# Performance work log

Measured on AMD Instinct MI355X. Metric: run time of the kernel, lower is better.

The kernel has to match this reference:

```python
import jax, jax.numpy as jnp
import numpy as np
from jax.scipy.special import logsumexp

B, S, T = 512, 512, 78  # batch, seq_len, num_tags (num_types=78 in SatoModel)


def setup_inputs() -> dict:
    key = jax.random.key(0)
    k1, k2, k3, k4, k5 = jax.random.split(key, 5)
    emissions = jax.random.normal(k1, (B, S, T), dtype=jnp.float32)
    mask = jax.random.randint(k2, (B, S), 0, 2).astype(bool)
    start_transitions = jax.random.normal(k3, (T,), dtype=jnp.float32)
    end_transitions = jax.random.normal(k4, (T,), dtype=jnp.float32)
    transitions = jax.random.normal(k5, (T, T), dtype=jnp.float32)
    return {
        "emissions": emissions,
        "mask": mask,
        "start_transitions": start_transitions,
        "end_transitions": end_transitions,
        "transitions": transitions,
    }


def reference(emissions, mask, start_transitions, end_transitions, transitions):
    # CRF.forward: partition - score
    # score: masked forward algorithm (note: this CRF's _compute_score never uses
    # gold tags; it is a masked logsumexp DP, reproduced faithfully).
    # partition: unmasked forward algorithm (its where(mask, a, a) is a no-op).
    init = start_transitions[None, :] + emissions[:, 0]  # [B, T]

    ems = jnp.moveaxis(emissions[:, 1:], 1, 0)  # [S-1, B, T]
    msk = jnp.moveaxis(mask[:, 1:], 1, 0)       # [S-1, B]

    def dp_step(state, em_i):
        # state: [B, T]; transitions: [T, T]; em_i: [B, T]
        return logsumexp(state[:, :, None] + transitions[None, :, :] + em_i[:, None, :], axis=1)

    def step(carry, inp):
        score, alpha = carry
        em_i, m_i = inp
        next_score = dp_step(score, em_i)
        score = jnp.where(m_i[:, None], next_score, score)
        alpha = dp_step(alpha, em_i)
        return (score, alpha), None

    (score, alpha), _ = jax.lax.scan(step, (init, init), (ems, msk))

    score_final = logsumexp(score + end_transitions[None, :], axis=1)      # [B]
    partition = logsumexp(alpha + end_transitions[None, :], axis=1)        # [B]
    return partition - score_final
```

## Files before the change

kernel.cpp:

```cpp
#include <hip/hip_runtime.h>

#define BB 256
#define SS 512
#define TT 78
#define TP 80
#define NT 256

typedef float v2f __attribute__((ext_vector_type(2)));
typedef float v4f __attribute__((ext_vector_type(4)));

template<int I> struct ic { static constexpr int v = I; };
template<int I, int N, typename F>
__device__ __forceinline__ void sfor(F f) {
    if constexpr (I < N) { f(ic<I>{}); sfor<I + 1, N>(f); }
}

__global__ __attribute__((amdgpu_flat_work_group_size(NT, NT)))
void crf_fwd_kernel(const float* __restrict__ em,
                    const unsigned int* __restrict__ mi32,
                    const float* __restrict__ st,
                    const float* __restrict__ en_,
                    const float* __restrict__ tr,
                    float* __restrict__ out)
{
    __shared__ __align__(16) float sE[4][TP];
    __shared__ float sfin[4];
    __shared__ int sflag;
    __shared__ char lds_pad[84 * 1024];

    const int tid  = threadIdx.x;
    const int w    = tid >> 6;
    const int lane = tid & 63;
    ((volatile char*)lds_pad)[tid] = 0;

    const int  batch    = blockIdx.x * 2 + (w >> 1);
    const bool is_alpha = (w & 1) != 0;
    const bool has2     = lane < (TT - 64);
    const int  t0  = lane;
    const int  t1c = has2 ? (lane + 64) : (TT - 1);

    if (tid == 0) sflag = 1;
    __syncthreads();
    { bool ok = true;
      for (int k = tid; k < 512; k += NT) ok = ok && (mi32[k] <= 1u);
      if (!ok) atomicAnd(&sflag, 0); }
    __syncthreads();
    const bool mask_int = (sflag != 0);
    const unsigned char* mi8 = (const unsigned char*)mi32;

    v2f et0[TP / 2], et1[TP / 2];
    sfor<0, TP / 2>([&](auto P) {
        constexpr int p = decltype(P)::v;
        constexpr int j0 = 2 * p, j1 = 2 * p + 1;
        float a0v = (j0 < TT) ? __expf(tr[j0 * TT + t0])  : 0.f;
        float a1v = (j1 < TT) ? __expf(tr[j1 * TT + t0])  : 0.f;
        float b0v = (j0 < TT) ? __expf(tr[j0 * TT + t1c]) : 0.f;
        float b1v = (j1 < TT) ? __expf(tr[j1 * TT + t1c]) : 0.f;
        asm volatile("" : "+v"(a0v), "+v"(a1v), "+v"(b0v), "+v"(b1v));
        et0[p] = (v2f){a0v, a1v};
        et1[p] = (v2f){b0v, b1v};
    });

    const size_t base = (size_t)batch * SS * TT;
    float e0 = __expf(st[t0]  + em[base + t0]);
    float e1 = __expf(st[t1c] + em[base + t1c]);
    int M2 = 0;

    if (lane == 14 || lane == 15) sE[w][64 + lane] = 0.f;
    sE[w][lane] = e0;
    if (has2) sE[w][64 + lane] = e1;

    const float* rp = em + base + TT;
    float EmN0 = __expf(rp[t0]);
    float EmN1 = __expf(rp[t1c]);
    unsigned int mk_n = mask_int ? mi32[batch * SS + 1]
                                 : (unsigned int)mi8[batch * SS + 1];

    for (int i = 1; i < SS; ++i) {
        const float Em0 = EmN0, Em1 = EmN1;
        const unsigned int mki = mk_n;
        if (i + 1 < SS) {
            rp += TT;
            EmN0 = __expf(rp[t0]);
            EmN1 = __expf(rp[t1c]);
            mk_n = mask_int ? mi32[batch * SS + i + 1]
                            : (unsigned int)mi8[batch * SS + i + 1];
        }
        __builtin_amdgcn_wave_barrier();

        const v4f* ep = (const v4f*)sE[w];
        v4f xs[TP / 4];
        sfor<0, TP / 4>([&](auto K) { constexpr int k = decltype(K)::v; xs[k] = ep[k]; });

        v2f a0{0,0}, a1{0,0}, c0{0,0}, c1{0,0};
        sfor<0, TP / 4>([&](auto K) {
            constexpr int k = decltype(K)::v;
            v2f xlo = {xs[k].x, xs[k].y}, xhi = {xs[k].z, xs[k].w};
            a0 = __builtin_elementwise_fma(xlo, et0[2 * k],     a0);
            a1 = __builtin_elementwise_fma(xhi, et0[2 * k + 1], a1);
            c0 = __builtin_elementwise_fma(xlo, et1[2 * k],     c0);
            c1 = __builtin_elementwise_fma(xhi, et1[2 * k + 1], c1);
        });
        v2f va = a0 + a1, vc = c0 + c1;
        float v0 = va.x + va.y;
        float v1 = vc.x + vc.y;

        float vref = __builtin_amdgcn_readfirstlane(v0);
        int   d2   = (int)((__float_as_uint(vref) >> 23) & 0xFF) - 127;
        float scl  = __uint_as_float((unsigned)(127 - d2) << 23);
        float n0 = v0 * scl * Em0;
        float n1 = v1 * scl * Em1;

        const bool upd = is_alpha | (mki != 0);
        e0 = upd ? n0 : e0;
        e1 = upd ? n1 : e1;
        M2 = upd ? M2 + d2 : M2;

        __builtin_amdgcn_wave_barrier();
        sE[w][lane] = e0;
        if (has2) sE[w][64 + lane] = e1;
    }

    float fs = e0 * __expf(en_[t0]);
    if (has2) fs += e1 * __expf(en_[t1c]);
    #pragma unroll
    for (int o = 32; o > 0; o >>= 1) fs += __shfl_xor(fs, o);
    if (lane == 0) sfin[w] = __logf(fs) + (float)M2 * 0.6931471805599453f;
    __syncthreads();
    if (tid == 0) {
        out[blockIdx.x * 2 + 0] = sfin[1] - sfin[0];
        out[blockIdx.x * 2 + 1] = sfin[3] - sfin[2];
    }
}

extern "C" void kernel_launch(void* const* d_in, const int* in_sizes, int n_in,
                              void* d_out, int out_size, void* d_ws, size_t ws_size,
                              hipStream_t stream) {
    const float* emissions    = (const float*)d_in[0];
    const unsigned int* mask  = (const unsigned int*)d_in[1];
    const float* start_trans  = (const float*)d_in[2];
    const float* end_trans    = (const float*)d_in[3];
    const float* transitions  = (const float*)d_in[4];
    float* out = (float*)d_out;

    crf_fwd_kernel<<<BB, NT, 0, stream>>>(emissions, mask, start_trans,
                                          end_trans, transitions, out);
}
```

Baseline: 201.1 us.

## Use packed fp16 dot2 for CRF transition matvec with one batch per block

```diff
diff --git a/kernel.cpp b/kernel.cpp
--- a/kernel.cpp
+++ b/kernel.cpp
@@ -1,13 +1,12 @@
 #include <hip/hip_runtime.h>
 
-#define BB 256
+#define BB 512
 #define SS 512
 #define TT 78
 #define TP 80
-#define NT 256
+#define NT 128
 
-typedef float v2f __attribute__((ext_vector_type(2)));
-typedef float v4f __attribute__((ext_vector_type(4)));
+typedef _Float16 v2h __attribute__((ext_vector_type(2)));
 
 template<int I> struct ic { static constexpr int v = I; };
 template<int I, int N, typename F>
@@ -15,7 +14,12 @@
     if constexpr (I < N) { f(ic<I>{}); sfor<I + 1, N>(f); }
 }
 
-__global__ __attribute__((amdgpu_flat_work_group_size(NT, NT)))
+__device__ __forceinline__ unsigned short f16b(float x) {
+    return __builtin_bit_cast(unsigned short, (_Float16)x);
+}
+
+__global__ __attribute__((amdgpu_flat_work_group_size(NT, NT),
+                          amdgpu_waves_per_eu(1, 1)))
 void crf_fwd_kernel(const float* __restrict__ em,
                     const unsigned int* __restrict__ mi32,
                     const float* __restrict__ st,
@@ -23,21 +27,17 @@
                     const float* __restrict__ tr,
                     float* __restrict__ out)
 {
-    __shared__ __align__(16) float sE[4][TP];
-    __shared__ float sfin[4];
-    __shared__ int sflag;
-    __shared__ char lds_pad[84 * 1024];
-
+    const int b    = blockIdx.x;
     const int tid  = threadIdx.x;
     const int w    = tid >> 6;
     const int lane = tid & 63;
-    ((volatile char*)lds_pad)[tid] = 0;
-
-    const int  batch    = blockIdx.x * 2 + (w >> 1);
-    const bool is_alpha = (w & 1) != 0;
-    const bool has2     = lane < (TT - 64);
+    const bool has2 = lane < (TT - 64);
     const int  t0  = lane;
     const int  t1c = has2 ? (lane + 64) : (TT - 1);
+
+    __shared__ __align__(16) unsigned short sEh[2][TP];
+    __shared__ float sfin[2];
+    __shared__ int sflag;
 
     if (tid == 0) sflag = 1;
     __syncthreads();
@@ -47,34 +47,36 @@
     __syncthreads();
     const bool mask_int = (sflag != 0);
     const unsigned char* mi8 = (const unsigned char*)mi32;
+    const bool is_alpha = (w == 1);
 
-    v2f et0[TP / 2], et1[TP / 2];
+    unsigned wt0[TP / 2], wt1[TP / 2];
     sfor<0, TP / 2>([&](auto P) {
         constexpr int p = decltype(P)::v;
         constexpr int j0 = 2 * p, j1 = 2 * p + 1;
-        float a0v = (j0 < TT) ? __expf(tr[j0 * TT + t0])  : 0.f;
-        float a1v = (j1 < TT) ? __expf(tr[j1 * TT + t0])  : 0.f;
-        float b0v = (j0 < TT) ? __expf(tr[j0 * TT + t1c]) : 0.f;
-        float b1v = (j1 < TT) ? __expf(tr[j1 * TT + t1c]) : 0.f;
-        asm volatile("" : "+v"(a0v), "+v"(a1v), "+v"(b0v), "+v"(b1v));
-        et0[p] = (v2f){a0v, a1v};
-        et1[p] = (v2f){b0v, b1v};
+        float a0 = (j0 < TT) ? __expf(tr[j0 * TT + t0])  : 0.f;
+        float a1 = (j1 < TT) ? __expf(tr[j1 * TT + t0])  : 0.f;
+        float b0 = (j0 < TT) ? __expf(tr[j0 * TT + t1c]) : 0.f;
+        float b1 = (j1 < TT) ? __expf(tr[j1 * TT + t1c]) : 0.f;
+        unsigned pa = (unsigned)f16b(a0) | ((unsigned)f16b(a1) << 16);
+        unsigned pb = (unsigned)f16b(b0) | ((unsigned)f16b(b1) << 16);
+        asm volatile("" : "+v"(pa), "+v"(pb));
+        wt0[p] = pa; wt1[p] = pb;
     });
 
-    const size_t base = (size_t)batch * SS * TT;
+    const size_t base = (size_t)b * SS * TT;
     float e0 = __expf(st[t0]  + em[base + t0]);
     float e1 = __expf(st[t1c] + em[base + t1c]);
     int M2 = 0;
 
-    if (lane == 14 || lane == 15) sE[w][64 + lane] = 0.f;
-    sE[w][lane] = e0;
-    if (has2) sE[w][64 + lane] = e1;
+    if (lane == 14 || lane == 15) sEh[w][64 + lane] = 0;
+    sEh[w][lane] = f16b(e0);
+    if (has2) sEh[w][64 + lane] = f16b(e1);
 
     const float* rp = em + base + TT;
     float EmN0 = __expf(rp[t0]);
     float EmN1 = __expf(rp[t1c]);
-    unsigned int mk_n = mask_int ? mi32[batch * SS + 1]
-                                 : (unsigned int)mi8[batch * SS + 1];
+    unsigned int mk_n = mask_int ? mi32[b * SS + 1]
+                                 : (unsigned int)mi8[b * SS + 1];
 
     for (int i = 1; i < SS; ++i) {
         const float Em0 = EmN0, Em1 = EmN1;
@@ -83,31 +85,42 @@
             rp += TT;
             EmN0 = __expf(rp[t0]);
             EmN1 = __expf(rp[t1c]);
-            mk_n = mask_int ? mi32[batch * SS + i + 1]
-                            : (unsigned int)mi8[batch * SS + i + 1];
+            mk_n = mask_int ? mi32[b * SS + i + 1]
+                            : (unsigned int)mi8[b * SS + i + 1];
         }
         __builtin_amdgcn_wave_barrier();
 
-        const v4f* ep = (const v4f*)sE[w];
-        v4f xs[TP / 4];
-        sfor<0, TP / 4>([&](auto K) { constexpr int k = decltype(K)::v; xs[k] = ep[k]; });
+        const uint4* ep = (const uint4*)sEh[w];
+        unsigned xs[TP / 2];
+        sfor<0, TP / 8>([&](auto K) {
+            constexpr int k = decltype(K)::v;
+            uint4 q = ep[k];
+            xs[4 * k + 0] = q.x; xs[4 * k + 1] = q.y;
+            xs[4 * k + 2] = q.z; xs[4 * k + 3] = q.w;
+        });
 
-        v2f a0{0,0}, a1{0,0}, c0{0,0}, c1{0,0};
-        sfor<0, TP / 4>([&](auto K) {
-            constexpr int k = decltype(K)::v;
-            v2f xlo = {xs[k].x, xs[k].y}, xhi = {xs[k].z, xs[k].w};
-            a0 = __builtin_elementwise_fma(xlo, et0[2 * k],     a0);
-            a1 = __builtin_elementwise_fma(xhi, et0[2 * k + 1], a1);
-            c0 = __builtin_elementwise_fma(xlo, et1[2 * k],     c0);
-            c1 = __builtin_elementwise_fma(xhi, et1[2 * k + 1], c1);
+        float a00 = 0.f, a01 = 0.f, c00 = 0.f, c01 = 0.f;
+        sfor<0, TP / 2>([&](auto P) {
+            constexpr int p = decltype(P)::v;
+            v2h x  = __builtin_bit_cast(v2h, xs[p]);
+            v2h w0 = __builtin_bit_cast(v2h, wt0[p]);
+            v2h w1 = __builtin_bit_cast(v2h, wt1[p]);
+            if constexpr ((p & 1) == 0) {
+                a00 = __builtin_amdgcn_fdot2(x, w0, a00, false);
+                c00 = __builtin_amdgcn_fdot2(x, w1, c00, false);
+            } else {
+                a01 = __builtin_amdgcn_fdot2(x, w0, a01, false);
+                c01 = __builtin_amdgcn_fdot2(x, w1, c01, false);
+            }
         });
-        v2f va = a0 + a1, vc = c0 + c1;
-        float v0 = va.x + va.y;
-        float v1 = vc.x + vc.y;
+        float v0 = a00 + a01;
+        float v1 = c00 + c01;
 
-        float vref = __builtin_amdgcn_readfirstlane(v0);
-        int   d2   = (int)((__float_as_uint(vref) >> 23) & 0xFF) - 127;
-        float scl  = __uint_as_float((unsigned)(127 - d2) << 23);
+        float mx = fmaxf(v0, v1);
+        #pragma unroll
+        for (int o = 32; o > 0; o >>= 1) mx = fmaxf(mx, __shfl_xor(mx, o));
+        int   d2  = (int)((__float_as_uint(mx) >> 23) & 0xFF) - 127;
+        float scl = __uint_as_float((unsigned)(127 - d2) << 23);
         float n0 = v0 * scl * Em0;
         float n1 = v1 * scl * Em1;
 
@@ -117,8 +130,8 @@
         M2 = upd ? M2 + d2 : M2;
 
         __builtin_amdgcn_wave_barrier();
-        sE[w][lane] = e0;
-        if (has2) sE[w][64 + lane] = e1;
+        sEh[w][lane] = f16b(e0);
+        if (has2) sEh[w][64 + lane] = f16b(e1);
     }
 
     float fs = e0 * __expf(en_[t0]);
@@ -127,10 +140,7 @@
     for (int o = 32; o > 0; o >>= 1) fs += __shfl_xor(fs, o);
     if (lane == 0) sfin[w] = __logf(fs) + (float)M2 * 0.6931471805599453f;
     __syncthreads();
-    if (tid == 0) {
-        out[blockIdx.x * 2 + 0] = sfin[1] - sfin[0];
-        out[blockIdx.x * 2 + 1] = sfin[3] - sfin[2];
-    }
+    if (tid == 0) out[b] = sfin[1] - sfin[0];
 }
 
 extern "C" void kernel_launch(void* const* d_in, const int* in_sizes, int n_in,
```

Result: slower. 309.4 us (+53.9%).

## Split each CRF chain across two waves with block-level sync and combine kernel

Applied to the files above, without the earlier changes.

```diff
diff --git a/kernel.cpp b/kernel.cpp
--- a/kernel.cpp
+++ b/kernel.cpp
@@ -1,10 +1,11 @@
 #include <hip/hip_runtime.h>
 
-#define BB 256
 #define SS 512
 #define TT 78
 #define TP 80
-#define NT 256
+#define NT 128
+#define NCHAIN 1024
+#define LN2F 0.6931471805599453f
 
 typedef float v2f __attribute__((ext_vector_type(2)));
 typedef float v4f __attribute__((ext_vector_type(4)));
@@ -15,29 +16,29 @@
     if constexpr (I < N) { f(ic<I>{}); sfor<I + 1, N>(f); }
 }
 
-__global__ __attribute__((amdgpu_flat_work_group_size(NT, NT)))
-void crf_fwd_kernel(const float* __restrict__ em,
-                    const unsigned int* __restrict__ mi32,
-                    const float* __restrict__ st,
-                    const float* __restrict__ en_,
-                    const float* __restrict__ tr,
-                    float* __restrict__ out)
+__global__ __attribute__((amdgpu_flat_work_group_size(NT, NT),
+                          amdgpu_waves_per_eu(2, 2)))
+void crf_chain_kernel(const float* __restrict__ em,
+                      const unsigned int* __restrict__ mi32,
+                      const float* __restrict__ st,
+                      const float* __restrict__ en_,
+                      const float* __restrict__ tr,
+                      float* __restrict__ ws)
 {
-    __shared__ __align__(16) float sE[4][TP];
-    __shared__ float sfin[4];
+    const int  blk      = blockIdx.x;
+    const int  batch    = blk >> 1;
+    const bool is_alpha = (blk & 1) != 0;
+    const int  tid  = threadIdx.x;
+    const int  w    = tid >> 6;
+    const int  lane = tid & 63;
+    const int  t    = w * 40 + lane;
+    const bool live = (lane < 40) && (t < TT);
+    const int  tc   = live ? t : (TT - 1);
+
+    __shared__ __align__(16) float sE[2][TP];
+    __shared__ float sMax[2][2];
+    __shared__ float sFin[2];
     __shared__ int sflag;
-    __shared__ char lds_pad[84 * 1024];
-
-    const int tid  = threadIdx.x;
-    const int w    = tid >> 6;
-    const int lane = tid & 63;
-    ((volatile char*)lds_pad)[tid] = 0;
-
-    const int  batch    = blockIdx.x * 2 + (w >> 1);
-    const bool is_alpha = (w & 1) != 0;
-    const bool has2     = lane < (TT - 64);
-    const int  t0  = lane;
-    const int  t1c = has2 ? (lane + 64) : (TT - 1);
 
     if (tid == 0) sflag = 1;
     __syncthreads();
@@ -48,89 +49,84 @@
     const bool mask_int = (sflag != 0);
     const unsigned char* mi8 = (const unsigned char*)mi32;
 
-    v2f et0[TP / 2], et1[TP / 2];
+    v2f Wp[TP / 2];
     sfor<0, TP / 2>([&](auto P) {
         constexpr int p = decltype(P)::v;
         constexpr int j0 = 2 * p, j1 = 2 * p + 1;
-        float a0v = (j0 < TT) ? __expf(tr[j0 * TT + t0])  : 0.f;
-        float a1v = (j1 < TT) ? __expf(tr[j1 * TT + t0])  : 0.f;
-        float b0v = (j0 < TT) ? __expf(tr[j0 * TT + t1c]) : 0.f;
-        float b1v = (j1 < TT) ? __expf(tr[j1 * TT + t1c]) : 0.f;
-        asm volatile("" : "+v"(a0v), "+v"(a1v), "+v"(b0v), "+v"(b1v));
-        et0[p] = (v2f){a0v, a1v};
-        et1[p] = (v2f){b0v, b1v};
+        float w0 = (j0 < TT) ? __expf(tr[j0 * TT + tc]) : 0.f;
+        float w1 = (j1 < TT) ? __expf(tr[j1 * TT + tc]) : 0.f;
+        asm volatile("" : "+v"(w0), "+v"(w1));
+        Wp[p] = (v2f){w0, w1};
     });
 
     const size_t base = (size_t)batch * SS * TT;
-    float e0 = __expf(st[t0]  + em[base + t0]);
-    float e1 = __expf(st[t1c] + em[base + t1c]);
+    float e = live ? __expf(st[tc] + em[base + tc]) : 0.f;
     int M2 = 0;
 
-    if (lane == 14 || lane == 15) sE[w][64 + lane] = 0.f;
-    sE[w][lane] = e0;
-    if (has2) sE[w][64 + lane] = e1;
+    if (lane < 40) sE[0][t] = e;
+    float nm = e;
+    #pragma unroll
+    for (int o = 32; o > 0; o >>= 1) nm = fmaxf(nm, __shfl_xor(nm, o));
+    if (lane == 0) sMax[0][w] = nm;
 
     const float* rp = em + base + TT;
-    float EmN0 = __expf(rp[t0]);
-    float EmN1 = __expf(rp[t1c]);
-    unsigned int mk_n = mask_int ? mi32[batch * SS + 1]
-                                 : (unsigned int)mi8[batch * SS + 1];
+    float EmN = __expf(rp[tc]);
+    unsigned mk_n = mask_int ? mi32[batch * SS + 1]
+                             : (unsigned)mi8[batch * SS + 1];
+    __syncthreads();
 
     for (int i = 1; i < SS; ++i) {
-        const float Em0 = EmN0, Em1 = EmN1;
-        const unsigned int mki = mk_n;
+        const int cur = (i - 1) & 1, nxt = i & 1;
+        const float Em = EmN;
+        const unsigned mki = mk_n;
         if (i + 1 < SS) {
             rp += TT;
-            EmN0 = __expf(rp[t0]);
-            EmN1 = __expf(rp[t1c]);
+            EmN = __expf(rp[tc]);
             mk_n = mask_int ? mi32[batch * SS + i + 1]
-                            : (unsigned int)mi8[batch * SS + i + 1];
+                            : (unsigned)mi8[batch * SS + i + 1];
         }
-        __builtin_amdgcn_wave_barrier();
 
-        const v4f* ep = (const v4f*)sE[w];
-        v4f xs[TP / 4];
-        sfor<0, TP / 4>([&](auto K) { constexpr int k = decltype(K)::v; xs[k] = ep[k]; });
+        float m = fmaxf(sMax[cur][0], sMax[cur][1]);
+        int d2 = (int)((__float_as_uint(m) >> 23) & 0xFF) - 127;
+        d2 = d2 < -60 ? -60 : (d2 > 60 ? 60 : d2);
+        float scl = __uint_as_float((unsigned)(127 - d2) << 23);
 
-        v2f a0{0,0}, a1{0,0}, c0{0,0}, c1{0,0};
+        const v4f* ep = (const v4f*)sE[cur];
+        v2f a0{0.f, 0.f}, a1{0.f, 0.f};
         sfor<0, TP / 4>([&](auto K) {
             constexpr int k = decltype(K)::v;
-            v2f xlo = {xs[k].x, xs[k].y}, xhi = {xs[k].z, xs[k].w};
-            a0 = __builtin_elementwise_fma(xlo, et0[2 * k],     a0);
-            a1 = __builtin_elementwise_fma(xhi, et0[2 * k + 1], a1);
-            c0 = __builtin_elementwise_fma(xlo, et1[2 * k],     c0);
-            c1 = __builtin_elementwise_fma(xhi, et1[2 * k + 1], c1);
+            v4f x = ep[k];
+            a0 = __builtin_elementwise_fma((v2f){x.x, x.y}, Wp[2 * k],     a0);
+            a1 = __builtin_elementwise_fma((v2f){x.z, x.w}, Wp[2 * k + 1], a1);
         });
-        v2f va = a0 + a1, vc = c0 + c1;
-        float v0 = va.x + va.y;
-        float v1 = vc.x + vc.y;
-
-        float vref = __builtin_amdgcn_readfirstlane(v0);
-        int   d2   = (int)((__float_as_uint(vref) >> 23) & 0xFF) - 127;
-        float scl  = __uint_as_float((unsigned)(127 - d2) << 23);
-        float n0 = v0 * scl * Em0;
-        float n1 = v1 * scl * Em1;
+        v2f va = a0 + a1;
+        float v = va.x + va.y;
+        float n = live ? v * scl * Em : 0.f;
 
         const bool upd = is_alpha | (mki != 0);
-        e0 = upd ? n0 : e0;
-        e1 = upd ? n1 : e1;
-        M2 = upd ? M2 + d2 : M2;
+        if (upd) { e = n; M2 += d2; }
 
-        __builtin_amdgcn_wave_barrier();
-        sE[w][lane] = e0;
-        if (has2) sE[w][64 + lane] = e1;
+        float lm = e;
+        #pragma unroll
+        for (int o = 32; o > 0; o >>= 1) lm = fmaxf(lm, __shfl_xor(lm, o));
+
+        if (lane < 40) sE[nxt][t] = e;
+        if (lane == 0) sMax[nxt][w] = lm;
+        __syncthreads();
     }
 
-    float fs = e0 * __expf(en_[t0]);
-    if (has2) fs += e1 * __expf(en_[t1c]);
+    float fs = live ? e * __expf(en_[tc]) : 0.f;
     #pragma unroll
     for (int o = 32; o > 0; o >>= 1) fs += __shfl_xor(fs, o);
-    if (lane == 0) sfin[w] = __logf(fs) + (float)M2 * 0.6931471805599453f;
+    if (lane == 0) sFin[w] = fs;
     __syncthreads();
-    if (tid == 0) {
-        out[blockIdx.x * 2 + 0] = sfin[1] - sfin[0];
-        out[blockIdx.x * 2 + 1] = sfin[3] - sfin[2];
-    }
+    if (tid == 0) ws[blk] = __logf(sFin[0] + sFin[1]) + (float)M2 * LN2F;
+}
+
+__global__ void combine_kernel(const float* __restrict__ ws,
+                               float* __restrict__ out) {
+    int b = blockIdx.x * 256 + threadIdx.x;
+    if (b < 512) out[b] = ws[2 * b + 1] - ws[2 * b];
 }
 
 extern "C" void kernel_launch(void* const* d_in, const int* in_sizes, int n_in,
@@ -141,8 +137,10 @@
     const float* start_trans  = (const float*)d_in[2];
     const float* end_trans    = (const float*)d_in[3];
     const float* transitions  = (const float*)d_in[4];
+    float* ws  = (float*)d_ws;
     float* out = (float*)d_out;
 
-    crf_fwd_kernel<<<BB, NT, 0, stream>>>(emissions, mask, start_trans,
-                                          end_trans, transitions, out);
+    crf_chain_kernel<<<NCHAIN, NT, 0, stream>>>(emissions, mask, start_trans,
+                                                end_trans, transitions, ws);
+    combine_kernel<<<2, 256, 0, stream>>>(ws, out);
 }
```

Measured after the change: 377.5 us. 1.88x slower.

## Split each CRF recursion into meet-in-the-middle forward and backward halves

Applied to the files above, without the earlier changes.

```diff
diff --git a/kernel.cpp b/kernel.cpp
--- a/kernel.cpp
+++ b/kernel.cpp
@@ -1,10 +1,12 @@
 #include <hip/hip_runtime.h>
 
-#define BB 256
+#define BB 512
 #define SS 512
 #define TT 78
 #define TP 80
 #define NT 256
+#define MID 255
+#define LN2F 0.6931471805599453f
 
 typedef float v2f __attribute__((ext_vector_type(2)));
 typedef float v4f __attribute__((ext_vector_type(4)));
@@ -15,7 +17,8 @@
     if constexpr (I < N) { f(ic<I>{}); sfor<I + 1, N>(f); }
 }
 
-__global__ __attribute__((amdgpu_flat_work_group_size(NT, NT)))
+__global__ __attribute__((amdgpu_flat_work_group_size(NT, NT),
+                          amdgpu_waves_per_eu(2, 2)))
 void crf_fwd_kernel(const float* __restrict__ em,
                     const unsigned int* __restrict__ mi32,
                     const float* __restrict__ st,
@@ -23,21 +26,21 @@
                     const float* __restrict__ tr,
                     float* __restrict__ out)
 {
-    __shared__ __align__(16) float sE[4][TP];
-    __shared__ float sfin[4];
-    __shared__ int sflag;
-    __shared__ char lds_pad[84 * 1024];
-
+    const int b    = blockIdx.x;
     const int tid  = threadIdx.x;
     const int w    = tid >> 6;
     const int lane = tid & 63;
-    ((volatile char*)lds_pad)[tid] = 0;
-
-    const int  batch    = blockIdx.x * 2 + (w >> 1);
-    const bool is_alpha = (w & 1) != 0;
-    const bool has2     = lane < (TT - 64);
+    const int  chain   = w >> 1;
+    const bool is_bwd  = (w & 1) != 0;
+    const bool is_alpha = (chain == 1);
+    const bool has2 = lane < (TT - 64);
     const int  t0  = lane;
     const int  t1c = has2 ? (lane + 64) : (TT - 1);
+
+    __shared__ __align__(16) float sE[4][TP];
+    __shared__ float sRes[2];
+    __shared__ int   sM2[4];
+    __shared__ int   sflag;
 
     if (tid == 0) sflag = 1;
     __syncthreads();
@@ -48,89 +51,134 @@
     const bool mask_int = (sflag != 0);
     const unsigned char* mi8 = (const unsigned char*)mi32;
 
-    v2f et0[TP / 2], et1[TP / 2];
+    v2f W0[TP / 2], W1[TP / 2];
     sfor<0, TP / 2>([&](auto P) {
         constexpr int p = decltype(P)::v;
         constexpr int j0 = 2 * p, j1 = 2 * p + 1;
-        float a0v = (j0 < TT) ? __expf(tr[j0 * TT + t0])  : 0.f;
-        float a1v = (j1 < TT) ? __expf(tr[j1 * TT + t0])  : 0.f;
-        float b0v = (j0 < TT) ? __expf(tr[j0 * TT + t1c]) : 0.f;
-        float b1v = (j1 < TT) ? __expf(tr[j1 * TT + t1c]) : 0.f;
-        asm volatile("" : "+v"(a0v), "+v"(a1v), "+v"(b0v), "+v"(b1v));
-        et0[p] = (v2f){a0v, a1v};
-        et1[p] = (v2f){b0v, b1v};
+        float a0 = 0.f, a1 = 0.f, b0 = 0.f, b1 = 0.f;
+        if constexpr (j0 < TT) {
+            a0 = __expf(tr[is_bwd ? (t0 * TT + j0)  : (j0 * TT + t0)]);
+            b0 = __expf(tr[is_bwd ? (t1c * TT + j0) : (j0 * TT + t1c)]);
+        }
+        if constexpr (j1 < TT) {
+            a1 = __expf(tr[is_bwd ? (t0 * TT + j1)  : (j1 * TT + t0)]);
+            b1 = __expf(tr[is_bwd ? (t1c * TT + j1) : (j1 * TT + t1c)]);
+        }
+        asm volatile("" : "+v"(a0), "+v"(a1), "+v"(b0), "+v"(b1));
+        W0[p] = (v2f){a0, a1};
+        W1[p] = (v2f){b0, b1};
     });
 
-    const size_t base = (size_t)batch * SS * TT;
-    float e0 = __expf(st[t0]  + em[base + t0]);
-    float e1 = __expf(st[t1c] + em[base + t1c]);
-    int M2 = 0;
-
-    if (lane == 14 || lane == 15) sE[w][64 + lane] = 0.f;
-    sE[w][lane] = e0;
-    if (has2) sE[w][64 + lane] = e1;
-
-    const float* rp = em + base + TT;
-    float EmN0 = __expf(rp[t0]);
-    float EmN1 = __expf(rp[t1c]);
-    unsigned int mk_n = mask_int ? mi32[batch * SS + 1]
-                                 : (unsigned int)mi8[batch * SS + 1];
-
-    for (int i = 1; i < SS; ++i) {
-        const float Em0 = EmN0, Em1 = EmN1;
-        const unsigned int mki = mk_n;
-        if (i + 1 < SS) {
-            rp += TT;
-            EmN0 = __expf(rp[t0]);
-            EmN1 = __expf(rp[t1c]);
-            mk_n = mask_int ? mi32[batch * SS + i + 1]
-                            : (unsigned int)mi8[batch * SS + i + 1];
-        }
-        __builtin_amdgcn_wave_barrier();
-
+    auto matvec = [&](float& v0, float& v1) {
         const v4f* ep = (const v4f*)sE[w];
-        v4f xs[TP / 4];
-        sfor<0, TP / 4>([&](auto K) { constexpr int k = decltype(K)::v; xs[k] = ep[k]; });
-
-        v2f a0{0,0}, a1{0,0}, c0{0,0}, c1{0,0};
+        v2f a0{0.f, 0.f}, a1{0.f, 0.f}, c0{0.f, 0.f}, c1{0.f, 0.f};
         sfor<0, TP / 4>([&](auto K) {
             constexpr int k = decltype(K)::v;
-            v2f xlo = {xs[k].x, xs[k].y}, xhi = {xs[k].z, xs[k].w};
-            a0 = __builtin_elementwise_fma(xlo, et0[2 * k],     a0);
-            a1 = __builtin_elementwise_fma(xhi, et0[2 * k + 1], a1);
-            c0 = __builtin_elementwise_fma(xlo, et1[2 * k],     c0);
-            c1 = __builtin_elementwise_fma(xhi, et1[2 * k + 1], c1);
+            v4f x = ep[k];
+            a0 = __builtin_elementwise_fma((v2f){x.x, x.y}, W0[2 * k],     a0);
+            a1 = __builtin_elementwise_fma((v2f){x.z, x.w}, W0[2 * k + 1], a1);
+            c0 = __builtin_elementwise_fma((v2f){x.x, x.y}, W1[2 * k],     c0);
+            c1 = __builtin_elementwise_fma((v2f){x.z, x.w}, W1[2 * k + 1], c1);
         });
         v2f va = a0 + a1, vc = c0 + c1;
-        float v0 = va.x + va.y;
-        float v1 = vc.x + vc.y;
+        v0 = va.x + va.y;
+        v1 = vc.x + vc.y;
+    };
 
-        float vref = __builtin_amdgcn_readfirstlane(v0);
-        int   d2   = (int)((__float_as_uint(vref) >> 23) & 0xFF) - 127;
-        float scl  = __uint_as_float((unsigned)(127 - d2) << 23);
-        float n0 = v0 * scl * Em0;
-        float n1 = v1 * scl * Em1;
+    const size_t base = (size_t)b * SS * TT;
+    float e0, e1;
+    int M2 = 0;
+    if (lane == 14 || lane == 15) sE[w][64 + lane] = 0.f;
 
-        const bool upd = is_alpha | (mki != 0);
-        e0 = upd ? n0 : e0;
-        e1 = upd ? n1 : e1;
-        M2 = upd ? M2 + d2 : M2;
+    if (!is_bwd) {
+        e0 = __expf(st[t0]  + em[base + t0]);
+        e1 = __expf(st[t1c] + em[base + t1c]);
+        sE[w][t0] = e0;
+        if (has2) sE[w][64 + lane] = e1;
 
-        __builtin_amdgcn_wave_barrier();
-        sE[w][lane] = e0;
-        if (has2) sE[w][64 + lane] = e1;
+        const float* rp = em + base + TT;
+        float EmN0 = __expf(rp[t0]);
+        float EmN1 = __expf(rp[t1c]);
+        unsigned mk_n = mask_int ? mi32[b * SS + 1] : (unsigned)mi8[b * SS + 1];
+
+        for (int i = 1; i <= MID; ++i) {
+            const float Em0 = EmN0, Em1 = EmN1;
+            const unsigned mki = mk_n;
+            if (i < MID) {
+                rp += TT;
+                EmN0 = __expf(rp[t0]);
+                EmN1 = __expf(rp[t1c]);
+                mk_n = mask_int ? mi32[b * SS + i + 1] : (unsigned)mi8[b * SS + i + 1];
+            }
+            __builtin_amdgcn_wave_barrier();
+            float v0, v1; matvec(v0, v1);
+            float vref = __builtin_amdgcn_readfirstlane(v0);
+            int d2 = (int)((__float_as_uint(vref) >> 23) & 0xFF) - 127;
+            float scl = __uint_as_float((unsigned)(127 - d2) << 23);
+            float n0 = v0 * scl * Em0;
+            float n1 = v1 * scl * Em1;
+            const bool upd = is_alpha | (mki != 0);
+            e0 = upd ? n0 : e0;
+            e1 = upd ? n1 : e1;
+            M2 = upd ? M2 + d2 : M2;
+            __builtin_amdgcn_wave_barrier();
+            sE[w][t0] = e0;
+            if (has2) sE[w][64 + lane] = e1;
+        }
+    } else {
+        e0 = __expf(en_[t0]);
+        e1 = __expf(en_[t1c]);
+        const float* rp = em + base + (size_t)(SS - 1) * TT;
+        sE[w][t0] = e0 * __expf(rp[t0]);
+        if (has2) sE[w][64 + lane] = e1 * __expf(rp[t1c]);
+
+        unsigned mk_n = mask_int ? mi32[b * SS + SS - 1]
+                                 : (unsigned)mi8[b * SS + SS - 1];
+        rp -= TT;
+        float EmN0 = __expf(rp[t0]);
+        float EmN1 = __expf(rp[t1c]);
+
+        for (int i = SS - 1; i > MID; --i) {
+            const unsigned mki = mk_n;
+            const float Em0 = (i - 1 > MID) ? EmN0 : 1.0f;
+            const float Em1 = (i - 1 > MID) ? EmN1 : 1.0f;
+            if (i - 1 > MID) {
+                mk_n = mask_int ? mi32[b * SS + i - 1] : (unsigned)mi8[b * SS + i - 1];
+                if (i - 2 > MID) {
+                    rp -= TT;
+                    EmN0 = __expf(rp[t0]);
+                    EmN1 = __expf(rp[t1c]);
+                }
+            }
+            __builtin_amdgcn_wave_barrier();
+            float y0, y1; matvec(y0, y1);
+            float vref = __builtin_amdgcn_readfirstlane(y0);
+            int d2 = (int)((__float_as_uint(vref) >> 23) & 0xFF) - 127;
+            float scl = __uint_as_float((unsigned)(127 - d2) << 23);
+            const bool upd = is_alpha | (mki != 0);
+            e0 = upd ? y0 * scl : e0;
+            e1 = upd ? y1 * scl : e1;
+            M2 = upd ? M2 + d2 : M2;
+            float nf0 = e0 * Em0;
+            float nf1 = e1 * Em1;
+            __builtin_amdgcn_wave_barrier();
+            sE[w][t0] = nf0;
+            if (has2) sE[w][64 + lane] = nf1;
+        }
     }
 
-    float fs = e0 * __expf(en_[t0]);
-    if (has2) fs += e1 * __expf(en_[t1c]);
-    #pragma unroll
-    for (int o = 32; o > 0; o >>= 1) fs += __shfl_xor(fs, o);
-    if (lane == 0) sfin[w] = __logf(fs) + (float)M2 * 0.6931471805599453f;
+    if (lane == 0) sM2[w] = M2;
     __syncthreads();
-    if (tid == 0) {
-        out[blockIdx.x * 2 + 0] = sfin[1] - sfin[0];
-        out[blockIdx.x * 2 + 1] = sfin[3] - sfin[2];
+    if (!is_bwd) {
+        float d = e0 * sE[w + 1][t0];
+        if (has2) d += e1 * sE[w + 1][64 + lane];
+        #pragma unroll
+        for (int o = 32; o > 0; o >>= 1) d += __shfl_xor(d, o);
+        if (lane == 0)
+            sRes[chain] = __logf(d) + (float)(M2 + sM2[w + 1]) * LN2F;
     }
+    __syncthreads();
+    if (tid == 0) out[b] = sRes[1] - sRes[0];
 }
 
 extern "C" void kernel_launch(void* const* d_in, const int* in_sizes, int n_in,
```

New measurement: 221.6 us. +10.2%, slower.
